# Kernel tuning notes

Hardware: AMD Instinct MI355X
Metric: run time of the kernel (lower is better)

The kernel has to match this reference:

```python
import jax, jax.numpy as jnp
import numpy as np

N = 100000          # nodes
E = 6400000         # edges (avg degree 64)
V0 = 1.0            # self.v0 (source assigns v0 despite u0 arg)
W0 = 1.0            # self.w0
EPS = 1e-12         # torch F.normalize eps


def setup_inputs() -> dict:
    key = jax.random.key(0)
    k1, k2, k3, k4 = jax.random.split(key, 4)
    return {
        "x": jax.random.normal(k1, (N, 1), dtype=jnp.float32),
        "theta": jax.random.normal(k2, (N, 1), dtype=jnp.float32),
        "edge_src": jax.random.randint(k3, (E,), 0, N, dtype=jnp.int64),
        "edge_dst": jax.random.randint(k4, (E,), 0, N, dtype=jnp.int64),
    }


def reference(x, theta, edge_src, edge_dst):
    # node velocity: v = v0 * [cos(theta), sin(theta)]  -> [N, 2]
    v = V0 * jnp.concatenate([jnp.cos(theta), jnp.sin(theta)], axis=-1)

    # per-edge message: dtheta = x[src] - theta[dst]; m = [cos, sin]  -> [E, 2]
    dtheta = x[edge_src] - theta[edge_dst]            # [E, 1]
    msg = jnp.concatenate([jnp.cos(dtheta), jnp.sin(dtheta)], axis=-1)  # [E, 2]

    # mailbox mean over incoming edges per dst node (segment mean)
    seg_sum = jax.ops.segment_sum(msg, edge_dst, num_segments=N)               # [N, 2]
    cnt = jax.ops.segment_sum(jnp.ones((E, 1), msg.dtype), edge_dst, num_segments=N)
    mean_cs = seg_sum / jnp.maximum(cnt, 1.0)

    # torque: w = w0 * normalize(mean_cs)[..., 1:2]  (L2-normalize, torch eps)
    norm = jnp.maximum(jnp.linalg.norm(mean_cs, axis=-1, keepdims=True), EPS)
    w = W0 * (mean_cs / norm)[..., 1:2]               # [N, 1]

    # updated ndata packed as [v_x, v_y, w]
    return jnp.concatenate([v, w], axis=-1)           # [N, 3]
```

## Files before the change

### kernel.cpp

```cpp
#include <hip/hip_runtime.h>
#include <math.h>


#define EPS 1e-12f
#define NPART 16
#define RNODES 6250
#define RMAX 6250
#define BLK 1024

#define NBIN 1024
#define BINBLK 512
#define CAP 512
#define BUF 512
#define OCAP 262144

static __device__ __forceinline__ unsigned long long pack_cs(float xv) {
    float sn, cs;
    __sincosf(xv, &sn, &cs);
    const int ci = __float2int_rn(cs * 32768.0f);
    const int si = __float2int_rn(sn * 32768.0f);
    return (1ull << 52)
         | ((unsigned long long)(unsigned)(si + 32768) << 26)
         | (unsigned long long)(unsigned)(ci + 32768);
}

__global__ __launch_bounds__(256) void prep_pack_kernel(
        const float* __restrict__ x,
        unsigned long long* __restrict__ pu, int N) {
    int i = blockIdx.x * blockDim.x + threadIdx.x;
    if (i < N) pu[i] = pack_cs(x[i]);
}

__global__ __launch_bounds__(BINBLK, 8) void bin_kernel(
        const float* __restrict__ x,
        const int* __restrict__ esrc,
        const int* __restrict__ edst,
        unsigned long long* __restrict__ pu,
        unsigned* __restrict__ records,
        int* __restrict__ counts,
        unsigned long long* __restrict__ oflow,
        int* __restrict__ oflow_cnt,
        int E, int N) {
    __shared__ unsigned stage[NPART * BUF];
    __shared__ int scur[NPART];

    {
        const int PPB = (N + NBIN) / NBIN;
        const int idx = blockIdx.x * PPB + threadIdx.x;
        if (threadIdx.x < PPB && idx <= N)
            pu[idx] = (idx < N) ? pack_cs(x[idx]) : 0ull;
    }
    if (threadIdx.x < NPART) scur[threadIdx.x] = 0;
    __syncthreads();

    const int chunk = (((E + NBIN - 1) / NBIN) + 7) & ~7;
    const int beg = blockIdx.x * chunk;
    const int end = min(beg + chunk, E);
    const int end8 = beg + (max(end - beg, 0) & ~7);
    unsigned* __restrict__ myrec =
        records + (size_t)blockIdx.x * (NPART * CAP);
    const int wave = threadIdx.x >> 6;
    const int lane = threadIdx.x & 63;

#define BIN_ONE(dd, ss) do {                                              \
        const unsigned d_ = (unsigned)(dd);                               \
        const unsigned p_ = d_ / RNODES;         \
        const unsigned dl_ = d_ - p_ * RNODES;         \
        const unsigned rec_ = ((unsigned)(ss) << 13) | dl_;               \
        const int slot_ = atomicAdd(&scur[p_], 1);                        \
        if (slot_ < BUF) {                                                \
            stage[p_ * BUF + slot_] = rec_;                               \
        } else {                                      \
            const int g_ = atomicAdd(oflow_cnt, 1);                       \
            if (g_ < OCAP)                                                \
                oflow[g_] = ((unsigned long long)(unsigned)(ss) << 32)    \
                          | d_;                                           \
        }                                                                 \
    } while (0)

    for (int i = beg + threadIdx.x * 8; i < end8; i += BINBLK * 8) {
        const int4 da = *(const int4*)&edst[i];
        const int4 db = *(const int4*)&edst[i + 4];
        const int4 sa = *(const int4*)&esrc[i];
        const int4 sb = *(const int4*)&esrc[i + 4];
        BIN_ONE(da.x, sa.x);
        BIN_ONE(da.y, sa.y);
        BIN_ONE(da.z, sa.z);
        BIN_ONE(da.w, sa.w);
        BIN_ONE(db.x, sb.x);
        BIN_ONE(db.y, sb.y);
        BIN_ONE(db.z, sb.z);
        BIN_ONE(db.w, sb.w);
    }
    for (int i = end8 + threadIdx.x; i < end; i += BINBLK)
        BIN_ONE(edst[i], esrc[i]);
#undef BIN_ONE

    __syncthreads();
    #pragma unroll
    for (int q = 0; q < 2; ++q) {
        const int p = wave * 2 + q;
        const int sc = min(scur[p], (int)BUF);
        const int c8 = min((sc + 7) & ~7, (int)CAP);
        for (int k = lane; k < c8; k += 64)
            myrec[p * CAP + k] = (k < sc) ? stage[p * BUF + k]
                                          : ((unsigned)N << 13);
        if (lane == 0) counts[blockIdx.x * NPART + p] = c8;
    }
}

__global__ __launch_bounds__(BLK, 2) void accum_kernel(
        const unsigned long long* __restrict__ pu,
        const unsigned* __restrict__ records,
        const int* __restrict__ counts,
        const unsigned long long* __restrict__ oflow,
        const int* __restrict__ oflow_cnt,
        unsigned long long* __restrict__ partials,
        int nslice) {
    __shared__ unsigned long long lacc[RMAX];
    const int p = blockIdx.x / nslice;
    const int s = blockIdx.x % nslice;

    for (int k = threadIdx.x; k < RNODES; k += BLK) lacc[k] = 0ull;
    __syncthreads();

    const int wave = threadIdx.x >> 6;
    const int lane = threadIdx.x & 63;
    const int wstep = (BLK / 64) * nslice;

    const int c0 = s + wave * nslice;
    const int c1 = c0 + wstep;
    const int cnt0 = (c0 < NBIN) ? counts[c0 * NPART + p] : 0;
    const int cnt1 = (c1 < NBIN) ? counts[c1 * NPART + p] : 0;
    const unsigned* __restrict__ b0 =
        records + ((size_t)(c0 * NPART + p)) * CAP + lane * 8;
    const unsigned* __restrict__ b1 =
        records + ((size_t)(c1 * NPART + p)) * CAP + lane * 8;
    const bool a0 = lane * 8 < cnt0;
    const bool a1 = lane * 8 < cnt1;
    uint4 ra0 = make_uint4(0, 0, 0, 0), rb0 = make_uint4(0, 0, 0, 0);
    uint4 ra1 = make_uint4(0, 0, 0, 0), rb1 = make_uint4(0, 0, 0, 0);
    if (a0) { ra0 = *(const uint4*)b0; rb0 = *(const uint4*)(b0 + 4); }
    if (a1) { ra1 = *(const uint4*)b1; rb1 = *(const uint4*)(b1 + 4); }

    if (a0) {
        const unsigned long long v0 = pu[ra0.x >> 13];
        const unsigned long long v1 = pu[ra0.y >> 13];
        const unsigned long long v2 = pu[ra0.z >> 13];
        const unsigned long long v3 = pu[ra0.w >> 13];
        const unsigned long long v4 = pu[rb0.x >> 13];
        const unsigned long long v5 = pu[rb0.y >> 13];
        const unsigned long long v6 = pu[rb0.z >> 13];
        const unsigned long long v7 = pu[rb0.w >> 13];
        atomicAdd(&lacc[ra0.x & 8191], v0);
        atomicAdd(&lacc[ra0.y & 8191], v1);
        atomicAdd(&lacc[ra0.z & 8191], v2);
        atomicAdd(&lacc[ra0.w & 8191], v3);
        atomicAdd(&lacc[rb0.x & 8191], v4);
        atomicAdd(&lacc[rb0.y & 8191], v5);
        atomicAdd(&lacc[rb0.z & 8191], v6);
        atomicAdd(&lacc[rb0.w & 8191], v7);
    }
    if (a1) {
        const unsigned long long v0 = pu[ra1.x >> 13];
        const unsigned long long v1 = pu[ra1.y >> 13];
        const unsigned long long v2 = pu[ra1.z >> 13];
        const unsigned long long v3 = pu[ra1.w >> 13];
        const unsigned long long v4 = pu[rb1.x >> 13];
        const unsigned long long v5 = pu[rb1.y >> 13];
        const unsigned long long v6 = pu[rb1.z >> 13];
        const unsigned long long v7 = pu[rb1.w >> 13];
        atomicAdd(&lacc[ra1.x & 8191], v0);
        atomicAdd(&lacc[ra1.y & 8191], v1);
        atomicAdd(&lacc[ra1.z & 8191], v2);
        atomicAdd(&lacc[ra1.w & 8191], v3);
        atomicAdd(&lacc[rb1.x & 8191], v4);
        atomicAdd(&lacc[rb1.y & 8191], v5);
        atomicAdd(&lacc[rb1.z & 8191], v6);
        atomicAdd(&lacc[rb1.w & 8191], v7);
    }

    if (s == 0) {
        const int oc = min(*oflow_cnt, (int)OCAP);
        const unsigned pBeg = (unsigned)(p * RNODES);
        for (int i = threadIdx.x; i < oc; i += BLK) {
            const unsigned long long e = oflow[i];
            const unsigned dl = (unsigned)e - pBeg;
            if (dl < (unsigned)RNODES) atomicAdd(&lacc[dl], pu[e >> 32]);
        }
    }

    __syncthreads();
    unsigned long long* dst = partials + (size_t)blockIdx.x * RNODES;
    for (int k = threadIdx.x; k < RNODES; k += BLK) dst[k] = lacc[k];
}

__global__ __launch_bounds__(BLK, 2) void scatter_kernel(
        const unsigned long long* __restrict__ pu,
        const int* __restrict__ esrc,
        const int* __restrict__ edst,
        unsigned long long* __restrict__ partials,
        int E, int R, int nslice) {
    __shared__ unsigned long long lacc[RMAX];
    const int p = blockIdx.x / nslice;
    const int s = blockIdx.x % nslice;
    const int pBeg = p * R;

    for (int k = threadIdx.x; k < R; k += BLK) lacc[k] = 0ull;
    __syncthreads();

    const int per = (((E + nslice - 1) / nslice) + 7) & ~7;
    const int beg = s * per;
    const int end = min(beg + per, E);
    const int end8 = beg + (max(end - beg, 0) & ~7);

    for (int i = beg + threadIdx.x * 8; i < end8; i += BLK * 8) {
        const int4 da = *(const int4*)&edst[i];
        const int4 db = *(const int4*)&edst[i + 4];
        const int4 sa = *(const int4*)&esrc[i];
        const int4 sb = *(const int4*)&esrc[i + 4];
        const unsigned dl0 = (unsigned)(da.x - pBeg);
        const unsigned dl1 = (unsigned)(da.y - pBeg);
        const unsigned dl2 = (unsigned)(da.z - pBeg);
        const unsigned dl3 = (unsigned)(da.w - pBeg);
        const unsigned dl4 = (unsigned)(db.x - pBeg);
        const unsigned dl5 = (unsigned)(db.y - pBeg);
        const unsigned dl6 = (unsigned)(db.z - pBeg);
        const unsigned dl7 = (unsigned)(db.w - pBeg);
        const bool h0 = dl0 < (unsigned)R, h1 = dl1 < (unsigned)R;
        const bool h2 = dl2 < (unsigned)R, h3 = dl3 < (unsigned)R;
        const bool h4 = dl4 < (unsigned)R, h5 = dl5 < (unsigned)R;
        const bool h6 = dl6 < (unsigned)R, h7 = dl7 < (unsigned)R;
        unsigned long long v0 = 0, v1 = 0, v2 = 0, v3 = 0;
        unsigned long long v4 = 0, v5 = 0, v6 = 0, v7 = 0;
        if (h0) v0 = pu[sa.x];
        if (h1) v1 = pu[sa.y];
        if (h2) v2 = pu[sa.z];
        if (h3) v3 = pu[sa.w];
        if (h4) v4 = pu[sb.x];
        if (h5) v5 = pu[sb.y];
        if (h6) v6 = pu[sb.z];
        if (h7) v7 = pu[sb.w];
        if (h0) atomicAdd(&lacc[dl0], v0);
        if (h1) atomicAdd(&lacc[dl1], v1);
        if (h2) atomicAdd(&lacc[dl2], v2);
        if (h3) atomicAdd(&lacc[dl3], v3);
        if (h4) atomicAdd(&lacc[dl4], v4);
        if (h5) atomicAdd(&lacc[dl5], v5);
        if (h6) atomicAdd(&lacc[dl6], v6);
        if (h7) atomicAdd(&lacc[dl7], v7);
    }
    for (int i = end8 + threadIdx.x; i < end; i += BLK) {
        const unsigned dl = (unsigned)(edst[i] - pBeg);
        if (dl < (unsigned)R) atomicAdd(&lacc[dl], pu[esrc[i]]);
    }

    __syncthreads();
    unsigned long long* dst = partials + (size_t)blockIdx.x * R;
    for (int k = threadIdx.x; k < R; k += BLK) dst[k] = lacc[k];
}

__global__ __launch_bounds__(256) void reduce_kernel(
        const float* __restrict__ theta,
        const unsigned long long* __restrict__ partials,
        float* __restrict__ out, int N, int R, int nslice) {
    const int n = blockIdx.x * blockDim.x + threadIdx.x;
    if (n >= N) return;
    const int p = n / R;
    const int j = n - p * R;
    const unsigned long long* base = partials + (size_t)p * nslice * R + j;
    unsigned long long t = 0ull;
    #pragma unroll 16
    for (int s = 0; s < nslice; ++s) t += base[(size_t)s * R];
    const long long k  = (long long)(t >> 52);
    const long long cf = (long long)(t & 0x3FFFFFFull);
    const long long sf = (long long)((t >> 26) & 0x3FFFFFFull);
    const float C  = (float)(cf - k * 32768) * (1.0f / 32768.0f);
    const float Sv = (float)(sf - k * 32768) * (1.0f / 32768.0f);
    float sn, cs;
    __sincosf(theta[n], &sn, &cs);
    const float nrm = fmaxf(sqrtf(C * C + Sv * Sv), EPS);
    out[3 * n + 0] = cs;
    out[3 * n + 1] = sn;
    out[3 * n + 2] = (cs * Sv - sn * C) / nrm;
}

__global__ __launch_bounds__(256) void prep_acc_kernel(float2* __restrict__ acc, int N) {
    int i = blockIdx.x * blockDim.x + threadIdx.x;
    if (i < N) acc[i] = make_float2(0.0f, 0.0f);
}

__global__ __launch_bounds__(256) void edge_scatter_sincos_kernel(
        const int* __restrict__ esrc,
        const int* __restrict__ edst,
        const float* __restrict__ x,
        float2* __restrict__ acc, int E) {
    const int i = (blockIdx.x * 256 + threadIdx.x) * 4;
    float* accf = (float*)acc;
    for (int k = i; k < min(i + 4, E); ++k) {
        float sn, cs;
        __sincosf(x[esrc[k]], &sn, &cs);
        const int d = edst[k];
        unsafeAtomicAdd(&accf[2 * d],     cs);
        unsafeAtomicAdd(&accf[2 * d + 1], sn);
    }
}

__global__ __launch_bounds__(256) void node_kernel(
        const float* __restrict__ theta,
        const float2* __restrict__ acc,
        float* __restrict__ out, int N) {
    int n = blockIdx.x * blockDim.x + threadIdx.x;
    if (n >= N) return;
    float sn, cs;
    __sincosf(theta[n], &sn, &cs);
    const float2 a = acc[n];
    const float nrm = fmaxf(sqrtf(a.x * a.x + a.y * a.y), EPS);
    out[3 * n + 0] = cs;
    out[3 * n + 1] = sn;
    out[3 * n + 2] = (cs * a.y - sn * a.x) / nrm;
}

extern "C" void kernel_launch(void* const* d_in, const int* in_sizes, int n_in,
                              void* d_out, int out_size, void* d_ws, size_t ws_size,
                              hipStream_t stream) {
    const float* x     = (const float*)d_in[0];
    const float* theta = (const float*)d_in[1];
    const int*   esrc  = (const int*)d_in[2];
    const int*   edst  = (const int*)d_in[3];
    float*       out   = (float*)d_out;

    const int N = in_sizes[0];
    const int E = in_sizes[2];

    if (N <= NPART * RNODES && N < (1 << 19)
        && (size_t)(N + 1) <= (size_t)NBIN * BINBLK) {
        const int nslice = 32;
        const size_t part_bytes = (size_t)NPART * nslice * RNODES * 8ull;
        const size_t pu_bytes   = (((size_t)(N + 1) * 8ull) + 15) & ~(size_t)15;
        const size_t rec_bytes  = (size_t)NBIN * NPART * CAP * 4ull;
        const size_t cnt_bytes  = (size_t)NBIN * NPART * 4ull;
        const size_t ofc_bytes  = 64;
        const size_t ofl_bytes  = (size_t)OCAP * 8ull;
        const size_t total = part_bytes + pu_bytes + rec_bytes + cnt_bytes
                           + ofc_bytes + ofl_bytes;
        if (ws_size >= total) {
            char* w = (char*)d_ws;
            unsigned long long* partials = (unsigned long long*)w; w += part_bytes;
            unsigned long long* pu       = (unsigned long long*)w; w += pu_bytes;
            unsigned*           records  = (unsigned*)w;           w += rec_bytes;
            int*                counts   = (int*)w;                w += cnt_bytes;
            int*                oflow_cnt= (int*)w;                w += ofc_bytes;
            unsigned long long* oflow    = (unsigned long long*)w;

            hipMemsetAsync(oflow_cnt, 0, sizeof(int), stream);
            bin_kernel<<<NBIN, BINBLK, 0, stream>>>(
                x, esrc, edst, pu, records, counts, oflow, oflow_cnt, E, N);
            accum_kernel<<<NPART * nslice, BLK, 0, stream>>>(
                pu, records, counts, oflow, oflow_cnt, partials, nslice);
            reduce_kernel<<<(N + 255) / 256, 256, 0, stream>>>(
                theta, partials, out, N, RNODES, nslice);
            return;
        }
    }

    {
        const int R = (N + NPART - 1) / NPART;
        const size_t pu_bytes = (size_t)N * sizeof(unsigned long long);
        if (R <= RMAX) {
            for (int nslice : {32, 16, 8}) {
                const size_t part_bytes =
                    (size_t)NPART * nslice * R * sizeof(unsigned long long);
                if (ws_size >= part_bytes + pu_bytes) {
                    unsigned long long* partials = (unsigned long long*)d_ws;
                    unsigned long long* pu =
                        (unsigned long long*)((char*)d_ws + part_bytes);
                    prep_pack_kernel<<<(N + 255) / 256, 256, 0, stream>>>(
                        x, pu, N);
                    scatter_kernel<<<NPART * nslice, BLK, 0, stream>>>(
                        pu, esrc, edst, partials, E, R, nslice);
                    reduce_kernel<<<(N + 255) / 256, 256, 0, stream>>>(
                        theta, partials, out, N, R, nslice);
                    return;
                }
            }
        }
    }

    float2* acc = (float2*)d_ws;
    prep_acc_kernel<<<(N + 255) / 256, 256, 0, stream>>>(acc, N);
    edge_scatter_sincos_kernel<<<(E + 1023) / 1024, 256, 0, stream>>>(esrc, edst, x, acc, E);
    node_kernel<<<(N + 255) / 256, 256, 0, stream>>>(theta, acc, out, N);
}
```

Measured before the change: 137.3 us.

## Split bin counters into sub-counters and replace partials reduce with global atomics

The binning stage now uses four sub-counters per partition, selected by thread group, to cut shared-memory atomic contention on each counter. It compacts the sub-buffers when writing records and sends any beyond capacity to the overflow list. The accumulate stage no longer writes per-slice partial arrays for a separate reduce kernel. It atomically adds nonzero packed sums into one zero-initialised per-node accumulator, and a light final kernel decodes it. This removes a large partials write and read but adds global 64-bit atomics and a bigger memset.

```diff
diff --git a/kernel.cpp b/kernel.cpp
--- a/kernel.cpp
+++ b/kernel.cpp
@@ -11,7 +11,8 @@
 #define NBIN 1024
 #define BINBLK 512
 #define CAP 512
-#define BUF 512
+#define NSUB 4
+#define SUBCAP 144
 #define OCAP 262144
 
 static __device__ __forceinline__ unsigned long long pack_cs(float xv) {
@@ -41,8 +42,8 @@
         unsigned long long* __restrict__ oflow,
         int* __restrict__ oflow_cnt,
         int E, int N) {
-    __shared__ unsigned stage[NPART * BUF];
-    __shared__ int scur[NPART];
+    __shared__ unsigned stage[NPART * NSUB * SUBCAP];
+    __shared__ int scur[NPART * NSUB];
 
     {
         const int PPB = (N + NBIN) / NBIN;
@@ -50,7 +51,7 @@
         if (threadIdx.x < PPB && idx <= N)
             pu[idx] = (idx < N) ? pack_cs(x[idx]) : 0ull;
     }
-    if (threadIdx.x < NPART) scur[threadIdx.x] = 0;
+    if (threadIdx.x < NPART * NSUB) scur[threadIdx.x] = 0;
     __syncthreads();
 
     const int chunk = (((E + NBIN - 1) / NBIN) + 7) & ~7;
@@ -61,15 +62,17 @@
         records + (size_t)blockIdx.x * (NPART * CAP);
     const int wave = threadIdx.x >> 6;
     const int lane = threadIdx.x & 63;
+    const int sub = (threadIdx.x >> 4) & (NSUB - 1);
 
 #define BIN_ONE(dd, ss) do {                                              \
         const unsigned d_ = (unsigned)(dd);                               \
         const unsigned p_ = d_ / RNODES;         \
         const unsigned dl_ = d_ - p_ * RNODES;         \
         const unsigned rec_ = ((unsigned)(ss) << 13) | dl_;               \
-        const int slot_ = atomicAdd(&scur[p_], 1);                        \
-        if (slot_ < BUF) {                                                \
-            stage[p_ * BUF + slot_] = rec_;                               \
+        const unsigned ci_ = p_ * NSUB + sub;      \
+        const int slot_ = atomicAdd(&scur[ci_], 1);                       \
+        if (slot_ < SUBCAP) {                                             \
+            stage[ci_ * SUBCAP + slot_] = rec_;                           \
         } else {                                      \
             const int g_ = atomicAdd(oflow_cnt, 1);                       \
             if (g_ < OCAP)                                                \
@@ -100,11 +103,35 @@
     #pragma unroll
     for (int q = 0; q < 2; ++q) {
         const int p = wave * 2 + q;
-        const int sc = min(scur[p], (int)BUF);
-        const int c8 = min((sc + 7) & ~7, (int)CAP);
-        for (int k = lane; k < c8; k += 64)
-            myrec[p * CAP + k] = (k < sc) ? stage[p * BUF + k]
-                                          : ((unsigned)N << 13);
+        int bc[NSUB], off[NSUB];
+        int total = 0;
+        #pragma unroll
+        for (int s4 = 0; s4 < NSUB; ++s4) {
+            bc[s4] = min(scur[p * NSUB + s4], (int)SUBCAP);
+            off[s4] = total;
+            total += bc[s4];
+        }
+        #pragma unroll
+        for (int s4 = 0; s4 < NSUB; ++s4) {
+            const unsigned* __restrict__ src =
+                stage + (p * NSUB + s4) * SUBCAP;
+            for (int k = lane; k < bc[s4]; k += 64) {
+                const int pos = off[s4] + k;
+                const unsigned rec = src[k];
+                if (pos < CAP) {
+                    myrec[p * CAP + pos] = rec;
+                } else {
+                    const int g = atomicAdd(oflow_cnt, 1);
+                    if (g < OCAP)
+                        oflow[g] = ((unsigned long long)(rec >> 13) << 32)
+                                 | (unsigned)(p * RNODES + (rec & 8191u));
+                }
+            }
+        }
+        const int wr = min(total, (int)CAP);
+        const int c8 = min((wr + 7) & ~7, (int)CAP);
+        for (int k = wr + lane; k < c8; k += 64)
+            myrec[p * CAP + k] = ((unsigned)N << 13);
         if (lane == 0) counts[blockIdx.x * NPART + p] = c8;
     }
 }
@@ -115,7 +142,7 @@
         const int* __restrict__ counts,
         const unsigned long long* __restrict__ oflow,
         const int* __restrict__ oflow_cnt,
-        unsigned long long* __restrict__ partials,
+        unsigned long long* __restrict__ acc,
         int nslice) {
     __shared__ unsigned long long lacc[RMAX];
     const int p = blockIdx.x / nslice;
@@ -191,8 +218,31 @@
     }
 
     __syncthreads();
-    unsigned long long* dst = partials + (size_t)blockIdx.x * RNODES;
-    for (int k = threadIdx.x; k < RNODES; k += BLK) dst[k] = lacc[k];
+    unsigned long long* __restrict__ accp = acc + (size_t)p * RNODES;
+    for (int k = threadIdx.x; k < RNODES; k += BLK) {
+        const unsigned long long v = lacc[k];
+        if (v) atomicAdd(&accp[k], v);
+    }
+}
+
+__global__ __launch_bounds__(256) void final_kernel(
+        const float* __restrict__ theta,
+        const unsigned long long* __restrict__ acc,
+        float* __restrict__ out, int N) {
+    const int n = blockIdx.x * blockDim.x + threadIdx.x;
+    if (n >= N) return;
+    const unsigned long long t = acc[n];
+    const long long k  = (long long)(t >> 52);
+    const long long cf = (long long)(t & 0x3FFFFFFull);
+    const long long sf = (long long)((t >> 26) & 0x3FFFFFFull);
+    const float C  = (float)(cf - k * 32768) * (1.0f / 32768.0f);
+    const float Sv = (float)(sf - k * 32768) * (1.0f / 32768.0f);
+    float sn, cs;
+    __sincosf(theta[n], &sn, &cs);
+    const float nrm = fmaxf(sqrtf(C * C + Sv * Sv), EPS);
+    out[3 * n + 0] = cs;
+    out[3 * n + 1] = sn;
+    out[3 * n + 2] = (cs * Sv - sn * C) / nrm;
 }
 
 __global__ __launch_bounds__(BLK, 2) void scatter_kernel(
@@ -336,30 +386,30 @@
     if (N <= NPART * RNODES && N < (1 << 19)
         && (size_t)(N + 1) <= (size_t)NBIN * BINBLK) {
         const int nslice = 32;
-        const size_t part_bytes = (size_t)NPART * nslice * RNODES * 8ull;
+        const size_t acc_bytes  = (size_t)NPART * RNODES * 8ull;
+        const size_t ofc_bytes  = 64;
         const size_t pu_bytes   = (((size_t)(N + 1) * 8ull) + 15) & ~(size_t)15;
         const size_t rec_bytes  = (size_t)NBIN * NPART * CAP * 4ull;
         const size_t cnt_bytes  = (size_t)NBIN * NPART * 4ull;
-        const size_t ofc_bytes  = 64;
         const size_t ofl_bytes  = (size_t)OCAP * 8ull;
-        const size_t total = part_bytes + pu_bytes + rec_bytes + cnt_bytes
-                           + ofc_bytes + ofl_bytes;
+        const size_t total = acc_bytes + ofc_bytes + pu_bytes + rec_bytes
+                           + cnt_bytes + ofl_bytes;
         if (ws_size >= total) {
             char* w = (char*)d_ws;
-            unsigned long long* partials = (unsigned long long*)w; w += part_bytes;
+            unsigned long long* acc      = (unsigned long long*)w; w += acc_bytes;
+            int*                oflow_cnt= (int*)w;                w += ofc_bytes;
             unsigned long long* pu       = (unsigned long long*)w; w += pu_bytes;
             unsigned*           records  = (unsigned*)w;           w += rec_bytes;
             int*                counts   = (int*)w;                w += cnt_bytes;
-            int*                oflow_cnt= (int*)w;                w += ofc_bytes;
             unsigned long long* oflow    = (unsigned long long*)w;
 
-            hipMemsetAsync(oflow_cnt, 0, sizeof(int), stream);
+            hipMemsetAsync(acc, 0, acc_bytes + ofc_bytes, stream);
             bin_kernel<<<NBIN, BINBLK, 0, stream>>>(
                 x, esrc, edst, pu, records, counts, oflow, oflow_cnt, E, N);
             accum_kernel<<<NPART * nslice, BLK, 0, stream>>>(
-                pu, records, counts, oflow, oflow_cnt, partials, nslice);
-            reduce_kernel<<<(N + 255) / 256, 256, 0, stream>>>(
-                theta, partials, out, N, RNODES, nslice);
+                pu, records, counts, oflow, oflow_cnt, acc, nslice);
+            final_kernel<<<(N + 255) / 256, 256, 0, stream>>>(
+                theta, acc, out, N);
             return;
         }
     }
```

Measured after the change: 147.0 us. +7.1%, slower.
